# Kernel tuning notes

Hardware: AMD Instinct MI355X
Metric: run time of the kernel (lower is better)

The kernel has to match this reference:

```python
import jax, jax.numpy as jnp
import numpy as np

N = 40000      # nodes
D = 64         # nnodefeatures
DEG = 32       # avg in-degree
E = N * DEG    # edges
G = 200        # graphs in batch
ATT = 64       # attention_size
HID = 128      # cls_hidden_dim
NCLS = 6
NLAYERS = 3


def setup_inputs() -> dict:
    key = jax.random.key(0)
    ks = jax.random.split(key, 8)
    s = 0.05
    x = jax.random.normal(ks[0], (N, D), dtype=jnp.float32)
    row = jax.random.randint(ks[1], (E,), 0, N, dtype=jnp.int32)
    # every node appears as a target exactly DEG times -> no zero degrees
    col = jnp.repeat(jnp.arange(N, dtype=jnp.int32), DEG)
    edge_index = jnp.stack([row, col])
    batch = jnp.repeat(jnp.arange(G, dtype=jnp.int32), N // G)
    W_lin = jax.random.normal(ks[2], (D, D), jnp.float32) * s
    b_lin = jnp.zeros((D,), jnp.float32)
    W_att = jax.random.normal(ks[3], (ATT, 2 * D), jnp.float32) * s
    a_vec = jnp.ones((ATT, 1), jnp.float32)  # torch.ones init
    W1 = jax.random.normal(ks[4], (HID, D), jnp.float32) * s
    b1 = jnp.zeros((HID,), jnp.float32)
    W2 = jax.random.normal(ks[5], (NCLS, HID), jnp.float32) * s
    b2 = jnp.zeros((NCLS,), jnp.float32)
    return dict(x=x, W_lin=W_lin, b_lin=b_lin, W_att=W_att, a_vec=a_vec,
                W1=W1, b1=b1, W2=W2, b2=b2,
                edge_index=edge_index, batch=batch, n_graphs=G)


def _gnn_layer(x, row, col, W_lin, b_lin, W_att, a_vec):
    n = x.shape[0]
    deg = jnp.sqrt(jax.ops.segment_sum(jnp.ones_like(col, dtype=x.dtype), col, num_segments=n))
    deg = jnp.where(jnp.isinf(deg), jnp.zeros_like(deg), deg)  # deg[deg==inf]=0
    norm = deg[row] * deg[col]                                  # [E]
    x_j = x[row]                                                # [E, D] gather source
    x_i = x[col]                                                # [E, D] gather target
    att_in = jnp.concatenate([x_j, x_i], axis=-1)               # [E, 2D]
    score = jnp.exp((att_in @ W_att.T) @ a_vec)                 # [E, 1]
    att_norm = jax.ops.segment_sum(score, col, num_segments=n)  # [N, 1] (scatter by edge_index[1])
    att = score / att_norm[row]                                 # gathered at edge_index[0] (faithful)
    m = ((x_j * att) @ W_lin.T + b_lin) / norm[:, None]         # [E, D]
    out = jax.ops.segment_sum(m, col, num_segments=n)           # aggregate by target
    return jax.nn.selu(out)


def reference(x, W_lin, b_lin, W_att, a_vec, W1, b1, W2, b2, edge_index, batch, n_graphs):
    row, col = edge_index[0], edge_index[1]
    # Faithful to original: the loop re-applies the layer to the ORIGINAL x each time
    for _ in range(NLAYERS):
        h = _gnn_layer(x, row, col, W_lin, b_lin, W_att, a_vec)
    sums = jax.ops.segment_sum(h, batch, num_segments=n_graphs)
    counts = jax.ops.segment_sum(jnp.ones((x.shape[0],), x.dtype), batch, num_segments=n_graphs)
    pooled = sums / counts[:, None]                              # global_mean_pool
    hcls = jax.nn.selu(pooled @ W1.T + b1)
    logits = hcls @ W2.T + b2
    return jax.nn.softmax(logits, axis=-1)
```

## Files before the change

### kernel.cpp

```cpp
#include <hip/hip_runtime.h>
#include <hip/hip_bf16.h>
#include <stdint.h>

#define N_NODES 40000
#define D_FEAT 64
#define DEG 32
#define E_EDGES (N_NODES * DEG)
#define G_GRAPHS 200
#define NPG 200
#define ATT_SZ 64
#define HID 128
#define NCLS 6
#define XS 69

__device__ __forceinline__ float selu_f(float x) {
    const float scale = 1.0507009873554805f;
    const float alpha = 1.6732632423543772f;
    return scale * (x > 0.f ? x : alpha * (__expf(x) - 1.f));
}

__device__ __forceinline__ uint32_t f2bf(float f) {
    uint32_t u = __builtin_bit_cast(uint32_t, f);
    return (u + 0x7fffu + ((u >> 16) & 1u)) >> 16;
}
__device__ __forceinline__ float bflo(uint32_t u) { return __builtin_bit_cast(float, u << 16); }
__device__ __forceinline__ float bfhi(uint32_t u) { return __builtin_bit_cast(float, u & 0xffff0000u); }

__global__ __launch_bounds__(256) void k_node(const float* __restrict__ x,
                                              const float* __restrict__ Wlin,
                                              const float* __restrict__ Watt,
                                              const float* __restrict__ avec,
                                              float* __restrict__ P,
                                              float* __restrict__ Q,
                                              uint32_t* __restrict__ yb,
                                              float* __restrict__ pool) {
    __shared__ float xs[160 * XS];
    __shared__ float ws[64 * XS];
    __shared__ float ws_w[128];
    int tid = threadIdx.x;
    int n0 = blockIdx.x * 160;
    if (blockIdx.x < 50) pool[blockIdx.x * 256 + tid] = 0.f;

    const float4* x4 = (const float4*)(x + (size_t)n0 * 64);
    const float4* W4 = (const float4*)Wlin;
#pragma unroll
    for (int s = 0; s < 10; ++s) {
        int idx = tid + s * 256, r = idx >> 4, kk = idx & 15;
        *(float4*)&xs[r * XS + kk * 4] = x4[idx];
    }
#pragma unroll
    for (int s = 0; s < 4; ++s) {
        int idx = tid + s * 256, r = idx >> 4, kk = idx & 15;
        *(float4*)&ws[r * XS + kk * 4] = W4[idx];
    }
    if (tid < 128) {
        float s = 0.f;
#pragma unroll
        for (int k = 0; k < ATT_SZ; ++k) s += avec[k] * Watt[k * 128 + tid];
        ws_w[tid] = s;
    }
    __syncthreads();

    if (tid < 160) {
        float s1 = 0.f, s2 = 0.f;
#pragma unroll 8
        for (int k = 0; k < 64; ++k) {
            float xv = xs[tid * XS + k];
            s1 += xv * ws_w[k];
            s2 += xv * ws_w[64 + k];
        }
        P[n0 + tid] = __expf(s1);
        Q[n0 + tid] = __expf(s2);
    }

    int tm = tid >> 4, tf = tid & 15;
    float acc[10][4];
#pragma unroll
    for (int i = 0; i < 10; ++i)
#pragma unroll
        for (int j = 0; j < 4; ++j) acc[i][j] = 0.f;
#pragma unroll 2
    for (int kk = 0; kk < 16; ++kk) {
        float4 wv[4];
#pragma unroll
        for (int j = 0; j < 4; ++j) wv[j] = *(const float4*)&ws[(4 * tf + j) * XS + kk * 4];
#pragma unroll
        for (int i = 0; i < 10; ++i) {
            float4 xv = *(const float4*)&xs[(tm + 16 * i) * XS + kk * 4];
#pragma unroll
            for (int j = 0; j < 4; ++j)
                acc[i][j] += xv.x * wv[j].x + xv.y * wv[j].y
                           + xv.z * wv[j].z + xv.w * wv[j].w;
        }
    }
#pragma unroll
    for (int i = 0; i < 10; ++i) {
        int m = n0 + tm + 16 * i;
        uint32_t p0 = f2bf(acc[i][0]) | (f2bf(acc[i][1]) << 16);
        uint32_t p1 = f2bf(acc[i][2]) | (f2bf(acc[i][3]) << 16);
        *(uint2*)&yb[(size_t)m * 32 + tf * 2] = make_uint2(p0, p1);
    }
}

__global__ __launch_bounds__(256) void k_edges(const int* __restrict__ row,
                                               const float* __restrict__ P,
                                               const float* __restrict__ Q,
                                               float* __restrict__ V) {
    int e = blockIdx.x * 256 + threadIdx.x;
    float p = P[row[e]];
#pragma unroll
    for (int off = 16; off; off >>= 1)
        p += __shfl_xor(p, off, 32);
    if ((threadIdx.x & 31) == 0) {
        int n = e >> 5;
        V[n] = P[n] / (Q[n] * p);
    }
}

__global__ __launch_bounds__(256) void k_agg(const int* __restrict__ row,
                                             const float* __restrict__ V,
                                             const float* __restrict__ Q,
                                             const uint32_t* __restrict__ yb,
                                             const float* __restrict__ blin,
                                             float* __restrict__ pool) {
    __shared__ float2 meta[1024];
    int tid = threadIdx.x;
    int n0 = blockIdx.x * 32;

    int4 r4 = ((const int4*)(row + (size_t)n0 * 32))[tid];
    meta[4 * tid + 0] = make_float2(V[r4.x], __builtin_bit_cast(float, r4.x << 7));
    meta[4 * tid + 1] = make_float2(V[r4.y], __builtin_bit_cast(float, r4.y << 7));
    meta[4 * tid + 2] = make_float2(V[r4.z], __builtin_bit_cast(float, r4.z << 7));
    meta[4 * tid + 3] = make_float2(V[r4.w], __builtin_bit_cast(float, r4.w << 7));
    __syncthreads();

    int wv = tid >> 6, lane = tid & 63;
    int q = lane >> 4, fi = lane & 15;
    float4 bl4 = ((const float4*)blin)[fi];
    int nw0 = n0 + wv * 8;
    float4 pacc = make_float4(0.f, 0.f, 0.f, 0.f);
    const char* ybc = (const char*)yb;
#pragma unroll 1
    for (int nn = 0; nn < 8; ++nn) {
        int n = nw0 + nn;
        int base = (wv * 8 + nn) * 32;
        float4 a = make_float4(0.f, 0.f, 0.f, 0.f);
#pragma unroll
        for (int s = 0; s < 8; ++s) {
            float2 m = meta[base + s * 4 + q];
            uint32_t rbyte = __builtin_bit_cast(uint32_t, m.y);
            uint2 u = *(const uint2*)(ybc + rbyte + fi * 8);
            a.x += m.x * bflo(u.x);
            a.y += m.x * bfhi(u.x);
            a.z += m.x * bflo(u.y);
            a.w += m.x * bfhi(u.y);
        }
        a.x += __shfl_xor(a.x, 16, 64); a.x += __shfl_xor(a.x, 32, 64);
        a.y += __shfl_xor(a.y, 16, 64); a.y += __shfl_xor(a.y, 32, 64);
        a.z += __shfl_xor(a.z, 16, 64); a.z += __shfl_xor(a.z, 32, 64);
        a.w += __shfl_xor(a.w, 16, 64); a.w += __shfl_xor(a.w, 32, 64);
        float qn = Q[n] * (1.f / 32.f);
        pacc.x += selu_f(qn * a.x + bl4.x);
        pacc.y += selu_f(qn * a.y + bl4.y);
        pacc.z += selu_f(qn * a.z + bl4.z);
        pacc.w += selu_f(qn * a.w + bl4.w);
    }
    if (q == 0) {
        int g = nw0 / NPG;
        float* pp = &pool[g * 64 + 4 * fi];
        atomicAdd(pp + 0, pacc.x);
        atomicAdd(pp + 1, pacc.y);
        atomicAdd(pp + 2, pacc.z);
        atomicAdd(pp + 3, pacc.w);
    }
}

__global__ __launch_bounds__(128) void k_cls(const float* __restrict__ pool,
                                             const float* __restrict__ W1,
                                             const float* __restrict__ b1,
                                             const float* __restrict__ W2,
                                             const float* __restrict__ b2,
                                             float* __restrict__ out) {
    __shared__ float ps[64];
    __shared__ float hc[HID];
    __shared__ float lg[NCLS];
    int t = threadIdx.x, g = blockIdx.x;
    if (t < 64) ps[t] = pool[g * 64 + t] * (1.f / NPG);
    __syncthreads();
    float s = b1[t];
    const float4* w14 = (const float4*)(W1 + t * 64);
    const float4* ps4 = (const float4*)ps;
#pragma unroll
    for (int kk = 0; kk < 16; ++kk) {
        float4 w = w14[kk], p = ps4[kk];
        s += w.x * p.x; s += w.y * p.y; s += w.z * p.z; s += w.w * p.w;
    }
    hc[t] = selu_f(s);
    __syncthreads();
    if (t < NCLS) {
        float l = b2[t];
        const float4* w24 = (const float4*)(W2 + t * 128);
        const float4* hc4 = (const float4*)hc;
        for (int kk = 0; kk < 32; ++kk) {
            float4 w = w24[kk], h = hc4[kk];
            l += w.x * h.x; l += w.y * h.y; l += w.z * h.z; l += w.w * h.w;
        }
        lg[t] = l;
    }
    __syncthreads();
    if (t == 0) {
        float m = lg[0];
        for (int c = 1; c < NCLS; ++c) m = fmaxf(m, lg[c]);
        float ex[NCLS], sum = 0.f;
        for (int c = 0; c < NCLS; ++c) { ex[c] = __expf(lg[c] - m); sum += ex[c]; }
        for (int c = 0; c < NCLS; ++c) out[g * NCLS + c] = ex[c] / sum;
    }
}

extern "C" void kernel_launch(void* const* d_in, const int* in_sizes, int n_in,
                              void* d_out, int out_size, void* d_ws, size_t ws_size,
                              hipStream_t stream) {
    const float* x    = (const float*)d_in[0];
    const float* Wlin = (const float*)d_in[1];
    const float* blin = (const float*)d_in[2];
    const float* Watt = (const float*)d_in[3];
    const float* avec = (const float*)d_in[4];
    const float* W1   = (const float*)d_in[5];
    const float* b1   = (const float*)d_in[6];
    const float* W2   = (const float*)d_in[7];
    const float* b2   = (const float*)d_in[8];
    const int*   row  = (const int*)d_in[9];
    float* out = (float*)d_out;

    float* P    = (float*)d_ws;
    float* Q    = P + N_NODES;
    float* V    = Q + N_NODES;
    float* pool = V + N_NODES;
    uint32_t* yb = (uint32_t*)(pool + G_GRAPHS * 64);

    k_node<<<N_NODES / 160, 256, 0, stream>>>(x, Wlin, Watt, avec, P, Q, yb, pool);
    k_edges<<<E_EDGES / 256, 256, 0, stream>>>(row, P, Q, V);
    k_agg<<<N_NODES / 32, 256, 0, stream>>>(row, V, Q, yb, blin, pool);
    k_cls<<<G_GRAPHS, 128, 0, stream>>>(pool, W1, b1, W2, b2, out);
}
```

Before: 130.2 us.

## Fuse classifier head into aggregation kernel via last-arriver atomic counter

Removes the separate classifier kernel launch. Each wave bumps a per-graph counter after adding its pooled partial sums, and the wave that completes a graph runs the MLP and softmax for that graph. Counters are zeroed in the node kernel. This saves one kernel launch and its tail, at the cost of a threadfence and an extra atomic per wave, plus serial classifier work done by a single wave inside the aggregation kernel.

```diff
diff --git a/kernel.cpp b/kernel.cpp
--- a/kernel.cpp
+++ b/kernel.cpp
@@ -33,13 +33,15 @@
                                               float* __restrict__ P,
                                               float* __restrict__ Q,
                                               uint32_t* __restrict__ yb,
-                                              float* __restrict__ pool) {
+                                              float* __restrict__ pool,
+                                              int* __restrict__ cnt) {
     __shared__ float xs[160 * XS];
     __shared__ float ws[64 * XS];
     __shared__ float ws_w[128];
     int tid = threadIdx.x;
     int n0 = blockIdx.x * 160;
     if (blockIdx.x < 50) pool[blockIdx.x * 256 + tid] = 0.f;
+    if (blockIdx.x == 50 && tid < G_GRAPHS) cnt[tid] = 0;
 
     const float4* x4 = (const float4*)(x + (size_t)n0 * 64);
     const float4* W4 = (const float4*)Wlin;
@@ -55,7 +57,6 @@
     }
     if (tid < 128) {
         float s = 0.f;
-#pragma unroll
         for (int k = 0; k < ATT_SZ; ++k) s += avec[k] * Watt[k * 128 + tid];
         ws_w[tid] = s;
     }
@@ -122,8 +123,17 @@
                                              const float* __restrict__ Q,
                                              const uint32_t* __restrict__ yb,
                                              const float* __restrict__ blin,
-                                             float* __restrict__ pool) {
+                                             float* __restrict__ pool,
+                                             int* __restrict__ cnt,
+                                             const float* __restrict__ W1,
+                                             const float* __restrict__ b1,
+                                             const float* __restrict__ W2,
+                                             const float* __restrict__ b2,
+                                             float* __restrict__ out) {
     __shared__ float2 meta[1024];
+    __shared__ float ps[4][64];
+    __shared__ float hcs[4][HID];
+    __shared__ float lgs[4][8];
     int tid = threadIdx.x;
     int n0 = blockIdx.x * 32;
 
@@ -165,55 +175,52 @@
         pacc.z += selu_f(qn * a.z + bl4.z);
         pacc.w += selu_f(qn * a.w + bl4.w);
     }
+    int g = nw0 / NPG;
     if (q == 0) {
-        int g = nw0 / NPG;
         float* pp = &pool[g * 64 + 4 * fi];
         atomicAdd(pp + 0, pacc.x);
         atomicAdd(pp + 1, pacc.y);
         atomicAdd(pp + 2, pacc.z);
         atomicAdd(pp + 3, pacc.w);
     }
-}
-
-__global__ __launch_bounds__(128) void k_cls(const float* __restrict__ pool,
-                                             const float* __restrict__ W1,
-                                             const float* __restrict__ b1,
-                                             const float* __restrict__ W2,
-                                             const float* __restrict__ b2,
-                                             float* __restrict__ out) {
-    __shared__ float ps[64];
-    __shared__ float hc[HID];
-    __shared__ float lg[NCLS];
-    int t = threadIdx.x, g = blockIdx.x;
-    if (t < 64) ps[t] = pool[g * 64 + t] * (1.f / NPG);
-    __syncthreads();
-    float s = b1[t];
-    const float4* w14 = (const float4*)(W1 + t * 64);
-    const float4* ps4 = (const float4*)ps;
-#pragma unroll
-    for (int kk = 0; kk < 16; ++kk) {
-        float4 w = w14[kk], p = ps4[kk];
-        s += w.x * p.x; s += w.y * p.y; s += w.z * p.z; s += w.w * p.w;
-    }
-    hc[t] = selu_f(s);
-    __syncthreads();
-    if (t < NCLS) {
-        float l = b2[t];
-        const float4* w24 = (const float4*)(W2 + t * 128);
-        const float4* hc4 = (const float4*)hc;
-        for (int kk = 0; kk < 32; ++kk) {
-            float4 w = w24[kk], h = hc4[kk];
-            l += w.x * h.x; l += w.y * h.y; l += w.z * h.z; l += w.w * h.w;
-        }
-        lg[t] = l;
-    }
-    __syncthreads();
-    if (t == 0) {
-        float m = lg[0];
-        for (int c = 1; c < NCLS; ++c) m = fmaxf(m, lg[c]);
-        float ex[NCLS], sum = 0.f;
-        for (int c = 0; c < NCLS; ++c) { ex[c] = __expf(lg[c] - m); sum += ex[c]; }
-        for (int c = 0; c < NCLS; ++c) out[g * NCLS + c] = ex[c] / sum;
+
+    __threadfence();
+    int old = 0;
+    if (lane == 0) old = atomicAdd(&cnt[g], 8);
+    old = __shfl(old, 0, 64);
+    if (old + 8 == NPG) {
+        float pv = atomicAdd(&pool[g * 64 + lane], 0.f);
+        ps[wv][lane] = pv * (1.f / NPG);
+        const float4* ps4 = (const float4*)ps[wv];
+#pragma unroll
+        for (int h = 0; h < 2; ++h) {
+            int t = lane + h * 64;
+            float s = b1[t];
+            const float4* w14 = (const float4*)(W1 + t * 64);
+#pragma unroll
+            for (int kk = 0; kk < 16; ++kk) {
+                float4 w = w14[kk], p = ps4[kk];
+                s += w.x * p.x; s += w.y * p.y; s += w.z * p.z; s += w.w * p.w;
+            }
+            hcs[wv][t] = selu_f(s);
+        }
+        if (lane < NCLS) {
+            float l = b2[lane];
+            const float4* w24 = (const float4*)(W2 + lane * 128);
+            const float4* hc4 = (const float4*)hcs[wv];
+            for (int kk = 0; kk < 32; ++kk) {
+                float4 w = w24[kk], h = hc4[kk];
+                l += w.x * h.x; l += w.y * h.y; l += w.z * h.z; l += w.w * h.w;
+            }
+            lgs[wv][lane] = l;
+        }
+        if (lane == 0) {
+            float m = lgs[wv][0];
+            for (int c = 1; c < NCLS; ++c) m = fmaxf(m, lgs[wv][c]);
+            float ex[NCLS], sum = 0.f;
+            for (int c = 0; c < NCLS; ++c) { ex[c] = __expf(lgs[wv][c] - m); sum += ex[c]; }
+            for (int c = 0; c < NCLS; ++c) out[g * NCLS + c] = ex[c] / sum;
+        }
     }
 }
 
@@ -236,10 +243,11 @@
     float* Q    = P + N_NODES;
     float* V    = Q + N_NODES;
     float* pool = V + N_NODES;
-    uint32_t* yb = (uint32_t*)(pool + G_GRAPHS * 64);
-
-    k_node<<<N_NODES / 160, 256, 0, stream>>>(x, Wlin, Watt, avec, P, Q, yb, pool);
+    int*   cnt  = (int*)(pool + G_GRAPHS * 64);
+    uint32_t* yb = (uint32_t*)(cnt + 256);
+
+    k_node<<<N_NODES / 160, 256, 0, stream>>>(x, Wlin, Watt, avec, P, Q, yb, pool, cnt);
     k_edges<<<E_EDGES / 256, 256, 0, stream>>>(row, P, Q, V);
-    k_agg<<<N_NODES / 32, 256, 0, stream>>>(row, V, Q, yb, blin, pool);
-    k_cls<<<G_GRAPHS, 128, 0, stream>>>(pool, W1, b1, W2, b2, out);
-}
+    k_agg<<<N_NODES / 32, 256, 0, stream>>>(row, V, Q, yb, blin, pool, cnt,
+                                            W1, b1, W2, b2, out);
+}
```

After: 247.7 us. +90.2%, slower.
